# Optimization experiments

Hardware: AMD Instinct MI355X
Metric: run time of the kernel (lower is better)

## Reference

```python
import jax, jax.numpy as jnp
import numpy as np

DIM = 512
WS = 7            # window size
N = WS * WS       # tokens per window
H = 16            # num heads
HD = DIM // H     # head dim
SCALE = HD ** -0.5
B_ = 2048         # batch * num_windows
NW = 64           # windows per image (mask leading dim)


def _relative_position_index():
    coords = np.stack(np.meshgrid(np.arange(WS), np.arange(WS), indexing='ij'))  # [2,WS,WS]
    cf = coords.reshape(2, -1)
    rel = cf[:, :, None] - cf[:, None, :]           # [2,N,N]
    rel = rel.transpose(1, 2, 0)
    rel[:, :, 0] += WS - 1
    rel[:, :, 1] += WS - 1
    rel[:, :, 0] *= 2 * WS - 1
    return rel.sum(-1).astype(np.int32)             # [N,N]

REL_IDX = _relative_position_index()


def setup_inputs() -> dict:
    key = jax.random.key(0)
    ks = jax.random.split(key, 7)
    return {
        'x': jax.random.normal(ks[0], (B_, N, DIM), jnp.float32),
        'mask': jax.random.normal(ks[1], (NW, N, N), jnp.float32),
        'qkv_w': jax.random.normal(ks[2], (DIM, 3 * DIM), jnp.float32) * 0.02,
        'qkv_b': jax.random.normal(ks[3], (3 * DIM,), jnp.float32) * 0.02,
        'proj_w': jax.random.normal(ks[4], (DIM, DIM), jnp.float32) * 0.02,
        'proj_b': jax.random.normal(ks[5], (DIM,), jnp.float32) * 0.02,
        'bias_table': jax.random.normal(ks[6], (169, H), jnp.float32) * 0.02,
    }


def reference(x, mask, qkv_w, qkv_b, proj_w, proj_b, bias_table):
    B, n, c = x.shape
    qkv = x @ qkv_w + qkv_b                              # [B,N,3C]
    qkv = qkv.reshape(B, n, 3, H, HD).transpose(2, 0, 3, 1, 4)  # [3,B,H,N,hd]
    q, k, v = qkv[0], qkv[1], qkv[2]
    attn = jnp.einsum('bhid,bhjd->bhij', q * SCALE, k)   # [B,H,N,N]
    # relative position bias gather: [N*N,H] -> [H,N,N]
    rel_bias = bias_table[REL_IDX.reshape(-1)].reshape(n, n, H).transpose(2, 0, 1)
    attn = attn + rel_bias[None]
    # shifted-window mask add: [B//nW, nW, H, N, N]
    attn = attn.reshape(B // NW, NW, H, n, n) + mask[None, :, None]
    attn = attn.reshape(B, H, n, n)
    attn = jax.nn.softmax(attn, axis=-1)
    out = jnp.einsum('bhij,bhjd->bhid', attn, v)         # [B,H,N,hd]
    out = out.transpose(0, 2, 1, 3).reshape(B, n, c)
    return out @ proj_w + proj_b
```

## Files before the change

kernel.cpp:

```cpp
#include <hip/hip_runtime.h>
#include <cstdint>

#define NTOK  49
#define NHEAD 16
#define HD    32
#define BATCH 2048
#define MTOT  (BATCH*NTOK)
#define SCALE 0.17677669529663687f

typedef float  f32x4  __attribute__((ext_vector_type(4)));
typedef __bf16 bf16x8 __attribute__((ext_vector_type(8)));
typedef __bf16 bf16x4 __attribute__((ext_vector_type(4)));
typedef unsigned int u32;
typedef const u32 __attribute__((address_space(1)))* gas_u32p;
typedef u32 __attribute__((address_space(3)))* las_u32p;

__device__ __forceinline__ void gld16(__bf16* lds, const __bf16* g) {
    __builtin_amdgcn_global_load_lds((gas_u32p)(const void*)g, (las_u32p)(void*)lds, 16, 0, 0);
}


__global__ __launch_bounds__(256) void cvt_x(const float* __restrict__ x,
                                             __bf16* __restrict__ o, long n) {
    long i = ((long)blockIdx.x * 256 + threadIdx.x) * 8;
    if (i >= n) return;
    float4 a = *(const float4*)(x + i);
    float4 b = *(const float4*)(x + i + 4);
    bf16x8 t;
    t[0] = (__bf16)a.x; t[1] = (__bf16)a.y; t[2] = (__bf16)a.z; t[3] = (__bf16)a.w;
    t[4] = (__bf16)b.x; t[5] = (__bf16)b.y; t[6] = (__bf16)b.z; t[7] = (__bf16)b.w;
    *(bf16x8*)(o + i) = t;
}

__global__ __launch_bounds__(256) void prep_w(const float* __restrict__ qkv_w,
                                              const float* __restrict__ proj_w,
                                              const float* __restrict__ qkv_b,
                                              __bf16* __restrict__ wqkv_t,
                                              __bf16* __restrict__ wp_t,
                                              float* __restrict__ qkvb_s) {
    int idx = blockIdx.x * 256 + threadIdx.x;
    if (idx < 1536 * 512) {
        int nn = idx >> 9, kk = idx & 511;
        float v = qkv_w[kk * 1536 + nn];
        if (nn < 512) v *= SCALE;
        wqkv_t[idx] = (__bf16)v;
    } else if (idx < 1536 * 512 + 512 * 512) {
        int j = idx - 1536 * 512;
        int nn = j >> 9, kk = j & 511;
        wp_t[j] = (__bf16)proj_w[kk * 512 + nn];
    } else if (idx < 1536 * 512 + 512 * 512 + 1536) {
        int n = idx - (1536 * 512 + 512 * 512);
        float v = qkv_b[n];
        if (n < 512) v *= SCALE;
        qkvb_s[n] = v;
    }
}

__global__ __launch_bounds__(256) void prep_addm(const float* __restrict__ mask,
                                                 const float* __restrict__ bias_table,
                                                 float* __restrict__ addm) {
    int idx = blockIdx.x * 256 + threadIdx.x;
    int rr   = idx & 3;
    int lane = (idx >> 2) & 63;
    int tile = (idx >> 8) & 15;
    int w    = (idx >> 12) & 63;
    int h    = idx >> 18;
    int mt = tile >> 2, nt = tile & 3;
    int g = lane >> 4, c = lane & 15;
    int i = mt * 16 + g * 4 + rr;
    int j = nt * 16 + c;
    float v;
    if (j >= 49)      v = -1e30f;
    else if (i >= 49) v = 0.f;
    else {
        int ai = (i * 37) >> 8, aj = i - ai * 7;
        int bi = (j * 37) >> 8, bj = j - bi * 7;
        int ridx = (ai - bi + 6) * 13 + (aj - bj + 6);
        v = bias_table[ridx * 16 + h] + mask[(w * 49 + i) * 49 + j];
    }
    addm[idx] = v;
}


#define WAIT8 asm volatile("s_waitcnt vmcnt(8)" ::: "memory")
#define WAIT4 asm volatile("s_waitcnt vmcnt(4)" ::: "memory")
#define WAIT0 asm volatile("s_waitcnt vmcnt(0)" ::: "memory")
#define BARR  do { asm volatile("s_barrier" ::: "memory"); \
                   __builtin_amdgcn_sched_barrier(0); } while (0)
#define NOOP  do {} while (0)

#define STAGE_A(sdb, skh, kc) do { \
    gld16(&Asm[sdb][skh][wid * 512],        Ag + (kc)); \
    gld16(&Asm[sdb][skh][4096 + wid * 512], Ag + 128 * 512 + (kc)); } while (0)
#define STAGE_B(sdb, skh, kc) do { \
    gld16(&Bsm[sdb][skh][wid * 512],        Bg + (kc)); \
    gld16(&Bsm[sdb][skh][4096 + wid * 512], Bg + 128 * 512 + (kc)); } while (0)

#define PHASE(db, kh, mh, STG, WT) do { \
    const __bf16* ab = &Asm[db][kh][(mh) ? aoff1 : aoff0]; \
    af[0] = *(const bf16x8*)(ab); \
    af[1] = *(const bf16x8*)(ab + 512); \
    af[2] = *(const bf16x8*)(ab + 1024); \
    af[3] = *(const bf16x8*)(ab + 1536); \
    if (!(mh)) { \
        const __bf16* bb = &Bsm[db][kh][boff]; \
        bfr[0] = *(const bf16x8*)(bb); \
        bfr[1] = *(const bf16x8*)(bb + 512); \
        bfr[2] = *(const bf16x8*)(bb + 1024); \
        bfr[3] = *(const bf16x8*)(bb + 1536); \
    } \
    STG; \
    WT; \
    BARR; \
    __builtin_amdgcn_s_setprio(1); \
    _Pragma("unroll") \
    for (int mf = 0; mf < 4; ++mf) { \
        _Pragma("unroll") \
        for (int nf = 0; nf < 4; ++nf) \
            acc[(mh) * 4 + mf][nf] = __builtin_amdgcn_mfma_f32_16x16x32_bf16( \
                af[mf], bfr[nf], acc[(mh) * 4 + mf][nf], 0, 0, 0); \
    } \
    __builtin_amdgcn_s_setprio(0); \
    __builtin_amdgcn_sched_barrier(0); \
  } while (0)

template <int MODE>
__global__ __launch_bounds__(512, 2)
void gemm256(const __bf16* __restrict__ A, const __bf16* __restrict__ Bt,
             const float* __restrict__ bias, float* __restrict__ outF,
             __bf16* __restrict__ outQK, __bf16* __restrict__ outVT, int NBX) {
    __shared__ __align__(16) __bf16 Asm[2][2][8192];
    __shared__ __align__(16) __bf16 Bsm[2][2][8192];
    const int tid  = threadIdx.x;
    const int wid  = tid >> 6;
    const int lane = tid & 63;
    const int g = lane >> 4, c = lane & 15;
    const int wr = wid >> 2, wc = wid & 3;

    const int nwg = NBX * 392;
    const int lin = blockIdx.y * NBX + blockIdx.x;
    const int sw  = (lin & 7) * (nwg >> 3) + (lin >> 3);
    const int bm  = sw / NBX;
    const int bn  = sw - bm * NBX;
    const long m0 = (long)bm * 256;
    const long n0 = (long)bn * 256;

    const int sr = tid >> 2;
    const int sl = (tid & 3) ^ ((tid >> 3) & 3);
    const __bf16* Ag = A  + (m0 + sr) * 512 + sl * 8;
    const __bf16* Bg = Bt + (n0 + sr) * 512 + sl * 8;

    const int koff  = (g ^ ((c >> 1) & 3)) * 8;
    const int aoff0 = (wr * 128 + c) * 32 + koff;
    const int aoff1 = aoff0 + 64 * 32;
    const int boff  = (wc * 64 + c) * 32 + koff;

    bf16x8 af[4], bfr[4];
    f32x4 acc[8][4];
#pragma unroll
    for (int i = 0; i < 8; ++i)
#pragma unroll
        for (int j = 0; j < 4; ++j) acc[i][j] = (f32x4){0.f, 0.f, 0.f, 0.f};

    STAGE_A(0, 0, 0);    STAGE_B(0, 0, 0);
    STAGE_A(0, 1, 32);   STAGE_B(0, 1, 32);
    STAGE_A(1, 0, 64);   STAGE_B(1, 0, 64);
    WAIT8;
    BARR;

#pragma unroll 1
    for (int t = 0; t < 6; ++t) {
        const int db = t & 1, odb = db ^ 1;
        const int kA = (t + 1) * 64 + 32;
        const int kB = (t + 2) * 64;
        PHASE(db, 0, 0, STAGE_A(odb, 1, kA), NOOP);
        PHASE(db, 0, 1, STAGE_B(odb, 1, kA), WAIT8);
        PHASE(db, 1, 0, STAGE_A(db, 0, kB),  NOOP);
        PHASE(db, 1, 1, STAGE_B(db, 0, kB),  WAIT8);
    }
    PHASE(0, 0, 0, STAGE_A(1, 1, 480), NOOP);
    PHASE(0, 0, 1, STAGE_B(1, 1, 480), WAIT8);
    PHASE(0, 1, 0, NOOP, NOOP);
    PHASE(0, 1, 1, NOOP, WAIT4);
    PHASE(1, 0, 0, NOOP, NOOP);
    PHASE(1, 0, 1, NOOP, WAIT0);
    PHASE(1, 1, 0, NOOP, NOOP);
    PHASE(1, 1, 1, NOOP, NOOP);

    if (MODE == 0) {
#pragma unroll
        for (int nf = 0; nf < 4; ++nf) {
            const int n = (int)n0 + wc * 64 + nf * 16 + c;
            const float bv = bias[n];
#pragma unroll
            for (int mi = 0; mi < 8; ++mi) {
                const long row0 = m0 + wr * 128 + mi * 16 + g * 4;
#pragma unroll
                for (int rr = 0; rr < 4; ++rr)
                    outF[(row0 + rr) * 512 + n] = acc[mi][nf][rr] + bv;
            }
        }
    } else if (n0 < 1024) {
#pragma unroll
        for (int nf = 0; nf < 4; ++nf) {
            const int n = (int)n0 + wc * 64 + nf * 16 + c;
            const float bv = bias[n];
#pragma unroll
            for (int mi = 0; mi < 8; ++mi) {
                const long row0 = m0 + wr * 128 + mi * 16 + g * 4;
#pragma unroll
                for (int rr = 0; rr < 4; ++rr)
                    outQK[(row0 + rr) * 1024 + n] = (__bf16)(acc[mi][nf][rr] + bv);
            }
        }
    } else {
#pragma unroll
        for (int nf = 0; nf < 4; ++nf) {
            const int n = (int)n0 + wc * 64 + nf * 16 + c;
            const float bv = bias[n];
            const int hh = (n - 1024) >> 5;
            const int dd = (n - 1024) & 31;
#pragma unroll
            for (int mi = 0; mi < 8; ++mi) {
                const int row0 = (int)m0 + wr * 128 + mi * 16 + g * 4;
#pragma unroll
                for (int rr = 0; rr < 4; ++rr) {
                    const int row = row0 + rr;
                    const int b2 = row / 49;
                    const int t2 = row - b2 * 49;
                    outVT[(long)(b2 * 512 + hh * 32 + dd) * 64 + t2] =
                        (__bf16)(acc[mi][nf][rr] + bv);
                }
            }
        }
    }
}


__global__ __launch_bounds__(256)
void attn_k(const __bf16* __restrict__ qk, const __bf16* __restrict__ vT,
            const float* __restrict__ addm, __bf16* __restrict__ ao) {
    __shared__ __bf16 p_all[4][64 * 72];
    const int tid = threadIdx.x;
    const int wid = tid >> 6;
    const int lane = tid & 63;
    const int g = lane >> 4, c = lane & 15;
    const int wv = blockIdx.x * 4 + wid;
    const int b = wv >> 4, h = wv & 15;
    const int w = b & 63;
    __bf16* psh = p_all[wid];

    const __bf16* base = qk + (long)b * 49 * 1024 + h * 32;

    bf16x8 zero8;
    for (int i = 0; i < 8; ++i) zero8[i] = (__bf16)0.f;

    bf16x8 aq[4], bk[4];
    for (int t4 = 0; t4 < 4; ++t4) {
        int t = t4 * 16 + c;
        const __bf16* p = base + (long)t * 1024 + g * 8;
        bool ok = t < 49;
        aq[t4] = ok ? *(const bf16x8*)p : zero8;
        bk[t4] = ok ? *(const bf16x8*)(p + 512) : zero8;
    }

    const float* am = addm + (long)(h * 64 + w) * 4096;
    f32x4 acc[4][4];
    for (int mt = 0; mt < 4; ++mt)
        for (int nt = 0; nt < 4; ++nt)
            acc[mt][nt] = *(const f32x4*)(am + (mt * 4 + nt) * 256 + lane * 4);

    for (int mt = 0; mt < 4; ++mt)
        for (int nt = 0; nt < 4; ++nt)
            acc[mt][nt] = __builtin_amdgcn_mfma_f32_16x16x32_bf16(aq[mt], bk[nt], acc[mt][nt], 0, 0, 0);

    float linv[4][4];
    for (int mt = 0; mt < 4; ++mt)
        for (int rr = 0; rr < 4; ++rr) {
            float mx = fmaxf(fmaxf(acc[mt][0][rr], acc[mt][1][rr]),
                             fmaxf(acc[mt][2][rr], acc[mt][3][rr]));
            for (int s = 1; s < 16; s <<= 1) mx = fmaxf(mx, __shfl_xor(mx, s));
            float sum = 0.f;
            for (int nt = 0; nt < 4; ++nt) {
                float p = __expf(acc[mt][nt][rr] - mx);
                acc[mt][nt][rr] = p;
                sum += p;
            }
            for (int s = 1; s < 16; s <<= 1) sum += __shfl_xor(sum, s);
            linv[mt][rr] = 1.0f / sum;
        }

    for (int mt = 0; mt < 4; ++mt)
        for (int nt = 0; nt < 4; ++nt)
            for (int rr = 0; rr < 4; ++rr)
                psh[(mt * 16 + g * 4 + rr) * 72 + nt * 16 + c] =
                    (__bf16)(acc[mt][nt][rr] * linv[mt][rr]);

    const __bf16* vb = vT + (long)(b * 16 + h) * 2048;
    bf16x8 av[2][2];
    for (int mt2 = 0; mt2 < 2; ++mt2)
        for (int k2 = 0; k2 < 2; ++k2)
            av[mt2][k2] = *(const bf16x8*)(vb + (mt2 * 16 + c) * 64 + k2 * 32 + g * 8);

    bf16x8 bp[4][2];
    for (int nt2 = 0; nt2 < 4; ++nt2)
        for (int k2 = 0; k2 < 2; ++k2)
            bp[nt2][k2] = *(const bf16x8*)(psh + (nt2 * 16 + c) * 72 + k2 * 32 + g * 8);

    f32x4 oacc[2][4];
    for (int mt2 = 0; mt2 < 2; ++mt2)
        for (int nt2 = 0; nt2 < 4; ++nt2) oacc[mt2][nt2] = (f32x4){0.f, 0.f, 0.f, 0.f};
    for (int mt2 = 0; mt2 < 2; ++mt2)
        for (int nt2 = 0; nt2 < 4; ++nt2)
            for (int k2 = 0; k2 < 2; ++k2)
                oacc[mt2][nt2] = __builtin_amdgcn_mfma_f32_16x16x32_bf16(av[mt2][k2], bp[nt2][k2], oacc[mt2][nt2], 0, 0, 0);

    __bf16* obase = ao + (long)b * 49 * 512 + h * 32;
    for (int nt2 = 0; nt2 < 4; ++nt2) {
        int i = nt2 * 16 + c;
        if (i < 49) {
            for (int mt2 = 0; mt2 < 2; ++mt2) {
                bf16x4 t;
                t[0] = (__bf16)oacc[mt2][nt2][0];
                t[1] = (__bf16)oacc[mt2][nt2][1];
                t[2] = (__bf16)oacc[mt2][nt2][2];
                t[3] = (__bf16)oacc[mt2][nt2][3];
                *(bf16x4*)(obase + (long)i * 512 + mt2 * 16 + g * 4) = t;
            }
        }
    }
}


extern "C" void kernel_launch(void* const* d_in, const int* in_sizes, int n_in,
                              void* d_out, int out_size, void* d_ws, size_t ws_size,
                              hipStream_t stream) {
    const float* x      = (const float*)d_in[0];
    const float* mask   = (const float*)d_in[1];
    const float* qkv_w  = (const float*)d_in[2];
    const float* qkv_b  = (const float*)d_in[3];
    const float* proj_w = (const float*)d_in[4];
    const float* proj_b = (const float*)d_in[5];
    const float* btab   = (const float*)d_in[6];
    float* out = (float*)d_out;

    char* ws = (char*)d_ws;
    __bf16* ws_x   = (__bf16*)ws;
    __bf16* ws_ao  = (__bf16*)ws;
    __bf16* ws_qk  = (__bf16*)(ws + 102760448L);
    __bf16* wqkv_t = (__bf16*)(ws + 308281344L);
    __bf16* wp_t   = (__bf16*)(ws + 309854208L);
    float*  qkvb_s = (float*)(ws + 310378496L);
    float*  addm   = (float*)(ws + 310384640L);
    __bf16* ws_vT  = (__bf16*)(ws + 327161856L);

    const long XN = (long)MTOT * 512;

    cvt_x<<<25088, 256, 0, stream>>>(x, ws_x, XN);
    prep_w<<<4102, 256, 0, stream>>>(qkv_w, proj_w, qkv_b, wqkv_t, wp_t, qkvb_s);
    prep_addm<<<16384, 256, 0, stream>>>(mask, btab, addm);

    gemm256<1><<<dim3(6, 392), 512, 0, stream>>>(ws_x, wqkv_t, qkvb_s, nullptr, ws_qk, ws_vT, 6);
    attn_k<<<8192, 256, 0, stream>>>(ws_qk, ws_vT, addm, ws_ao);
    gemm256<0><<<dim3(2, 392), 512, 0, stream>>>(ws_ao, wp_t, proj_b, out, nullptr, nullptr, 2);
}
```

Baseline: 905.3 us.

## Prefetch next LDS fragments into double registers during MFMA phases

```diff
diff --git a/kernel.cpp b/kernel.cpp
--- a/kernel.cpp
+++ b/kernel.cpp
@@ -96,31 +96,35 @@
     gld16(&Bsm[sdb][skh][wid * 512],        Bg + (kc)); \
     gld16(&Bsm[sdb][skh][4096 + wid * 512], Bg + 128 * 512 + (kc)); } while (0)
 
-#define PHASE(db, kh, mh, STG, WT) do { \
-    const __bf16* ab = &Asm[db][kh][(mh) ? aoff1 : aoff0]; \
-    af[0] = *(const bf16x8*)(ab); \
-    af[1] = *(const bf16x8*)(ab + 512); \
-    af[2] = *(const bf16x8*)(ab + 1024); \
-    af[3] = *(const bf16x8*)(ab + 1536); \
-    if (!(mh)) { \
-        const __bf16* bb = &Bsm[db][kh][boff]; \
-        bfr[0] = *(const bf16x8*)(bb); \
-        bfr[1] = *(const bf16x8*)(bb + 512); \
-        bfr[2] = *(const bf16x8*)(bb + 1024); \
-        bfr[3] = *(const bf16x8*)(bb + 1536); \
-    } \
+#define RD_A(DST, db, kh, mh) do { \
+    DST[0] = *(const bf16x8*)(aBase + (db)*16384 + (kh)*8192 + (mh)*2048); \
+    DST[1] = *(const bf16x8*)(aBase + (db)*16384 + (kh)*8192 + (mh)*2048 + 512); \
+    DST[2] = *(const bf16x8*)(aBase + (db)*16384 + (kh)*8192 + (mh)*2048 + 1024); \
+    DST[3] = *(const bf16x8*)(aBase + (db)*16384 + (kh)*8192 + (mh)*2048 + 1536); \
+  } while (0)
+#define RD_B(DST, db, kh) do { \
+    DST[0] = *(const bf16x8*)(bBase + (db)*16384 + (kh)*8192); \
+    DST[1] = *(const bf16x8*)(bBase + (db)*16384 + (kh)*8192 + 512); \
+    DST[2] = *(const bf16x8*)(bBase + (db)*16384 + (kh)*8192 + 1024); \
+    DST[3] = *(const bf16x8*)(bBase + (db)*16384 + (kh)*8192 + 1536); \
+  } while (0)
+
+#define PHASE(AX, mh, STG, WT, RPRE, RPOST) do { \
     STG; \
     WT; \
     BARR; \
+    RPRE; \
+    __builtin_amdgcn_sched_barrier(0); \
     __builtin_amdgcn_s_setprio(1); \
     _Pragma("unroll") \
     for (int mf = 0; mf < 4; ++mf) { \
         _Pragma("unroll") \
         for (int nf = 0; nf < 4; ++nf) \
             acc[(mh) * 4 + mf][nf] = __builtin_amdgcn_mfma_f32_16x16x32_bf16( \
-                af[mf], bfr[nf], acc[(mh) * 4 + mf][nf], 0, 0, 0); \
+                AX[mf], bfr[nf], acc[(mh) * 4 + mf][nf], 0, 0, 0); \
     } \
     __builtin_amdgcn_s_setprio(0); \
+    RPOST; \
     __builtin_amdgcn_sched_barrier(0); \
   } while (0)
 
@@ -151,11 +155,10 @@
     const __bf16* Bg = Bt + (n0 + sr) * 512 + sl * 8;
 
     const int koff  = (g ^ ((c >> 1) & 3)) * 8;
-    const int aoff0 = (wr * 128 + c) * 32 + koff;
-    const int aoff1 = aoff0 + 64 * 32;
-    const int boff  = (wc * 64 + c) * 32 + koff;
-
-    bf16x8 af[4], bfr[4];
+    const __bf16* aBase = &Asm[0][0][(wr * 128 + c) * 32 + koff];
+    const __bf16* bBase = &Bsm[0][0][(wc * 64 + c) * 32 + koff];
+
+    bf16x8 a0[4], a1[4], bfr[4];
     f32x4 acc[8][4];
 #pragma unroll
     for (int i = 0; i < 8; ++i)
@@ -167,25 +170,35 @@
     STAGE_A(1, 0, 64);   STAGE_B(1, 0, 64);
     WAIT8;
     BARR;
+    RD_A(a0, 0, 0, 0);
+    RD_B(bfr, 0, 0);
+    __builtin_amdgcn_sched_barrier(0);
 
 #pragma unroll 1
     for (int t = 0; t < 6; ++t) {
-        const int db = t & 1, odb = db ^ 1;
+        const int db = t & 1;
         const int kA = (t + 1) * 64 + 32;
         const int kB = (t + 2) * 64;
-        PHASE(db, 0, 0, STAGE_A(odb, 1, kA), NOOP);
-        PHASE(db, 0, 1, STAGE_B(odb, 1, kA), WAIT8);
-        PHASE(db, 1, 0, STAGE_A(db, 0, kB),  NOOP);
-        PHASE(db, 1, 1, STAGE_B(db, 0, kB),  WAIT8);
-    }
-    PHASE(0, 0, 0, STAGE_A(1, 1, 480), NOOP);
-    PHASE(0, 0, 1, STAGE_B(1, 1, 480), WAIT8);
-    PHASE(0, 1, 0, NOOP, NOOP);
-    PHASE(0, 1, 1, NOOP, WAIT4);
-    PHASE(1, 0, 0, NOOP, NOOP);
-    PHASE(1, 0, 1, NOOP, WAIT0);
-    PHASE(1, 1, 0, NOOP, NOOP);
-    PHASE(1, 1, 1, NOOP, NOOP);
+        if (db == 0) {
+            PHASE(a0, 0, STAGE_A(1, 1, kA), NOOP,  RD_A(a1, 0, 0, 1), NOOP);
+            PHASE(a1, 1, STAGE_B(1, 1, kA), WAIT8, RD_A(a0, 0, 1, 0), RD_B(bfr, 0, 1));
+            PHASE(a0, 0, STAGE_A(0, 0, kB), NOOP,  RD_A(a1, 0, 1, 1), NOOP);
+            PHASE(a1, 1, STAGE_B(0, 0, kB), WAIT8, RD_A(a0, 1, 0, 0), RD_B(bfr, 1, 0));
+        } else {
+            PHASE(a0, 0, STAGE_A(0, 1, kA), NOOP,  RD_A(a1, 1, 0, 1), NOOP);
+            PHASE(a1, 1, STAGE_B(0, 1, kA), WAIT8, RD_A(a0, 1, 1, 0), RD_B(bfr, 1, 1));
+            PHASE(a0, 0, STAGE_A(1, 0, kB), NOOP,  RD_A(a1, 1, 1, 1), NOOP);
+            PHASE(a1, 1, STAGE_B(1, 0, kB), WAIT8, RD_A(a0, 0, 0, 0), RD_B(bfr, 0, 0));
+        }
+    }
+    PHASE(a0, 0, STAGE_A(1, 1, 480), NOOP,  RD_A(a1, 0, 0, 1), NOOP);
+    PHASE(a1, 1, STAGE_B(1, 1, 480), WAIT8, RD_A(a0, 0, 1, 0), RD_B(bfr, 0, 1));
+    PHASE(a0, 0, NOOP, NOOP,  RD_A(a1, 0, 1, 1), NOOP);
+    PHASE(a1, 1, NOOP, WAIT4, RD_A(a0, 1, 0, 0), RD_B(bfr, 1, 0));
+    PHASE(a0, 0, NOOP, NOOP,  RD_A(a1, 1, 0, 1), NOOP);
+    PHASE(a1, 1, NOOP, WAIT0, RD_A(a0, 1, 1, 0), RD_B(bfr, 1, 1));
+    PHASE(a0, 0, NOOP, NOOP,  RD_A(a1, 1, 1, 1), NOOP);
+    PHASE(a1, 1, NOOP, NOOP,  NOOP, NOOP);
 
     if (MODE == 0) {
 #pragma unroll
```

Result: slower. 2.562 ms (+182.9%).
